# Performance work log

Hardware: AMD Instinct MI355X
Metric: run time of the kernel (lower is better)

## Reference

```python
import jax, jax.numpy as jnp
import numpy as np

B, T, L, D, H = 8, 8192, 256, 512, 8
HD = D // H  # head_dim = 64


def setup_inputs() -> dict:
    key = jax.random.key(0)
    ks = jax.random.split(key, 6)
    s = 0.02
    return {
        "x": jax.random.normal(ks[0], (B, T, D), jnp.float32),
        "query": jax.random.normal(ks[1], (B, L, D), jnp.float32),
        "Wq": jax.random.normal(ks[2], (D, D), jnp.float32) * s,
        "bq": jnp.zeros((D,), jnp.float32),
        "Wkv": jax.random.normal(ks[3], (D, 2 * D), jnp.float32) * s,
        "bkv": jnp.zeros((2 * D,), jnp.float32),
        "Wproj": jax.random.normal(ks[4], (D, D), jnp.float32) * s,
        "bproj": jnp.zeros((D,), jnp.float32),
    }


def reference(x, query, Wq, bq, Wkv, bkv, Wproj, bproj):
    scale = HD ** (-0.5)
    # projections (weights stored [in, out]; equivalent to torch Linear with W.T)
    q = (query @ Wq + bq).reshape(B, L, H, HD).transpose(0, 2, 1, 3)   # [B,H,L,hd]
    kv = (x @ Wkv + bkv).reshape(B, T, 2, H, HD)
    k = kv[:, :, 0].transpose(0, 2, 1, 3)                              # [B,H,T,hd]
    v = kv[:, :, 1].transpose(0, 2, 1, 3)                              # [B,H,T,hd]
    # scaled dot-product attention, full L x T scores as in original
    attn = jnp.einsum("bhld,bhtd->bhlt", q * scale, k)                 # [B,H,L,T]
    attn = jax.nn.softmax(attn, axis=-1)
    out = jnp.einsum("bhlt,bhtd->bhld", attn, v)                       # [B,H,L,hd]
    out = out.transpose(0, 2, 1, 3).reshape(B, L, D)
    return out @ Wproj + bproj
```

## Files before the change

kernel.cpp:

```cpp
#include <hip/hip_runtime.h>
#include <hip/hip_bf16.h>
#include <cstdint>
#include <cstddef>

typedef __bf16 bf16_t;
typedef __bf16 bf16x8 __attribute__((ext_vector_type(8)));
typedef __bf16 bf16x4 __attribute__((ext_vector_type(4)));
typedef float  f32x4  __attribute__((ext_vector_type(4)));

#define DEVI __device__ __forceinline__

constexpr int B_ = 8, T_ = 8192, L_ = 256, D_ = 512, H_ = 8, HD_ = 64;
constexpr float SCALE_LOG2E = 0.125f * 1.44269504088896340736f;
constexpr int NSPLIT = 8;

DEVI float fast_exp2(float x) {
#if __has_builtin(__builtin_amdgcn_exp2f)
  return __builtin_amdgcn_exp2f(x);
#else
  return exp2f(x);
#endif
}

DEVI void async16(void* lds_base, const void* gptr) {
#if __has_builtin(__builtin_amdgcn_global_load_lds)
  __builtin_amdgcn_global_load_lds(
      (__attribute__((address_space(1))) void*)gptr,
      (__attribute__((address_space(3))) void*)lds_base, 16, 0, 0);
#else
  ((bf16x8*)lds_base)[threadIdx.x & 63] = *(const bf16x8*)gptr;
#endif
}

__global__ __launch_bounds__(256) void cvt_f32_to_bf16(
    const float* __restrict__ in, bf16_t* __restrict__ out, int n4) {
  int stride = gridDim.x * blockDim.x;
  for (int i = blockIdx.x * blockDim.x + threadIdx.x; i < n4; i += stride) {
    float4 v = ((const float4*)in)[i];
    bf16x4 o;
    o[0] = (bf16_t)v.x; o[1] = (bf16_t)v.y; o[2] = (bf16_t)v.z; o[3] = (bf16_t)v.w;
    ((bf16x4*)out)[i] = o;
  }
}

__global__ __launch_bounds__(256) void transpose_cvt(
    const float* __restrict__ W, bf16_t* __restrict__ WT, int K, int N, float scale) {
  __shared__ float tile[32][33];
  const int tx = threadIdx.x & 31, ty = threadIdx.x >> 5;
  const int n0 = blockIdx.x * 32, k0 = blockIdx.y * 32;
#pragma unroll
  for (int i = 0; i < 4; ++i)
    tile[ty + i * 8][tx] = W[(size_t)(k0 + ty + i * 8) * N + n0 + tx];
  __syncthreads();
#pragma unroll
  for (int i = 0; i < 4; ++i)
    WT[(size_t)(n0 + ty + i * 8) * K + k0 + tx] = (bf16_t)(tile[tx][ty + i * 8] * scale);
}

template <int MODE>
__global__ __launch_bounds__(256, 4) void gemm_bf16(
    const bf16_t* __restrict__ A, const bf16_t* __restrict__ BT,
    const float* __restrict__ bias, float bscale,
    bf16_t* __restrict__ out0,
    float* __restrict__ outf) {
  constexpr int K = 512;
  __shared__ __align__(16) union SM {
    bf16_t stage[2][128 * 64];
    bf16_t cs[128 * 136];
  } sm;

  const int tid = threadIdx.x;
  const int w = tid >> 6, lane = tid & 63;
  const int m0 = blockIdx.x * 128, n0 = blockIdx.y * 128;
  const int wm = w & 1, wn = w >> 1;

  f32x4 acc[4][4] = {};

  const int sw = ((lane & 7) ^ ((lane >> 3) & 7)) * 8;
  const bf16_t* aG = A + (size_t)(m0 + w * 32 + (lane >> 3)) * K + sw;
  const bf16_t* bG = BT + (size_t)(n0 + w * 32 + (lane >> 3)) * K + sw;
  bf16_t* aL = &sm.stage[0][(w * 32) * 64];
  bf16_t* bL = &sm.stage[1][(w * 32) * 64];

  for (int k0 = 0; k0 < K; k0 += 64) {
#pragma unroll
    for (int i = 0; i < 4; ++i) {
      async16(aL + i * (8 * 64), aG + k0 + (size_t)(i * 8) * K);
      async16(bL + i * (8 * 64), bG + k0 + (size_t)(i * 8) * K);
    }
    __syncthreads();
#pragma unroll
    for (int kk = 0; kk < 2; ++kk) {
      bf16x8 af[4], bfr[4];
      const int cc = ((kk * 4 + (lane >> 4)) ^ (lane & 7)) * 8;
#pragma unroll
      for (int mt = 0; mt < 4; ++mt)
        af[mt] = *(const bf16x8*)&sm.stage[0][(wm * 64 + mt * 16 + (lane & 15)) * 64 + cc];
#pragma unroll
      for (int nt = 0; nt < 4; ++nt)
        bfr[nt] = *(const bf16x8*)&sm.stage[1][(wn * 64 + nt * 16 + (lane & 15)) * 64 + cc];
#pragma unroll
      for (int mt = 0; mt < 4; ++mt)
#pragma unroll
        for (int nt = 0; nt < 4; ++nt)
          acc[mt][nt] = __builtin_amdgcn_mfma_f32_16x16x32_bf16(af[mt], bfr[nt], acc[mt][nt], 0, 0, 0);
    }
    __syncthreads();
  }

  if (MODE == 2) {
#pragma unroll
    for (int nt = 0; nt < 4; ++nt) {
      const int col = n0 + wn * 64 + nt * 16 + (lane & 15);
      const float bv = bias[col];
#pragma unroll
      for (int mt = 0; mt < 4; ++mt)
#pragma unroll
        for (int r = 0; r < 4; ++r) {
          const int row = m0 + wm * 64 + mt * 16 + (lane >> 4) * 4 + r;
          outf[(size_t)row * D_ + col] = acc[mt][nt][r] + bv;
        }
    }
    return;
  }

#pragma unroll
  for (int nt = 0; nt < 4; ++nt) {
    const int col = wn * 64 + nt * 16 + (lane & 15);
    const float bv = bias[n0 + col] * bscale;
#pragma unroll
    for (int mt = 0; mt < 4; ++mt)
#pragma unroll
      for (int r = 0; r < 4; ++r) {
        const int row = wm * 64 + mt * 16 + (lane >> 4) * 4 + r;
        sm.cs[row * 136 + col] = (bf16_t)(acc[mt][nt][r] + bv);
      }
  }
  __syncthreads();

#pragma unroll
  for (int i = 0; i < 8; ++i) {
    const int c = tid + i * 256;
    const int row = c >> 4, col = (c & 15) * 8;
    const int gr = m0 + row;
    const int b = gr >> 8, l = gr & 255;
    const int h = (n0 + col) >> 6, hd = (n0 + col) & 63;
    *(float4*)&out0[((size_t)(b * 8 + h) * L_ + l) * 64 + hd] =
        *(const float4*)&sm.cs[row * 136 + col];
  }
}

__global__ __launch_bounds__(512, 2) void gemm_kv(
    const bf16_t* __restrict__ A, const bf16_t* __restrict__ BT,
    const float* __restrict__ bias,
    bf16_t* __restrict__ kh, bf16_t* __restrict__ vTh) {
  constexpr int K = 512;
  __shared__ __align__(16) union SM {
    bf16_t stage[2][2][256 * 64];
    bf16_t cs[128 * 264];
  } sm;

  const int tid = threadIdx.x;
  const int w = tid >> 6, lane = tid & 63;
  const int wm = w & 1, wn = w >> 1;

  const int b = blockIdx.x;
  const int xcd = b & 7, idx = b >> 3;
  const int m0 = ((xcd << 5) | (idx >> 2)) * 256;
  const int n0 = (idx & 3) * 256;

  f32x4 acc[8][4] = {};

  const int sw = ((lane & 7) ^ ((lane >> 3) & 7)) * 8;
  const int rl = w * 8 + (lane >> 3);
  const bf16_t* aG = A + (size_t)(m0 + rl) * K + sw;
  const bf16_t* bG = BT + (size_t)(n0 + rl) * K + sw;
  bf16_t* SS = &sm.stage[0][0][0];

  const int la = lane & 15;
  const int cc0 = ((lane >> 4) ^ (lane & 7)) * 8;
  const int cc1 = ((4 + (lane >> 4)) ^ (lane & 7)) * 8;

  bf16x8 ra[8], rb[4];

  auto stage_full = [&](int bufo, int k0) {
    bf16_t* dA = SS + bufo + (w * 8) * 64;
    bf16_t* dB = SS + bufo + 16384 + (w * 8) * 64;
#pragma unroll
    for (int i = 0; i < 4; ++i)
      async16(dA + i * 4096, aG + k0 + (size_t)(i * 64) * K);
#pragma unroll
    for (int i = 0; i < 4; ++i)
      async16(dB + i * 4096, bG + k0 + (size_t)(i * 64) * K);
  };
  auto ld_a = [&](const bf16_t* base, int mq) {
#pragma unroll
    for (int mt = 0; mt < 4; ++mt) {
      ra[mt * 2]     = *(const bf16x8*)&base[(mq * 64 + mt * 16 + la) * 64 + cc0];
      ra[mt * 2 + 1] = *(const bf16x8*)&base[(mq * 64 + mt * 16 + la) * 64 + cc1];
    }
  };
  auto ld_b = [&](const bf16_t* base, int nq) {
#pragma unroll
    for (int ntl = 0; ntl < 2; ++ntl) {
      rb[ntl * 2]     = *(const bf16x8*)&base[((nq * 2 + ntl) * 16 + la) * 64 + cc0];
      rb[ntl * 2 + 1] = *(const bf16x8*)&base[((nq * 2 + ntl) * 16 + la) * 64 + cc1];
    }
  };
  auto mm16 = [&](int mq, int nq) {
    __builtin_amdgcn_s_setprio(1);
#pragma unroll
    for (int mt = 0; mt < 4; ++mt)
#pragma unroll
      for (int ntl = 0; ntl < 2; ++ntl) {
        f32x4& c = acc[mq * 4 + mt][nq * 2 + ntl];
        c = __builtin_amdgcn_mfma_f32_16x16x32_bf16(ra[mt * 2],     rb[ntl * 2],     c, 0, 0, 0);
        c = __builtin_amdgcn_mfma_f32_16x16x32_bf16(ra[mt * 2 + 1], rb[ntl * 2 + 1], c, 0, 0, 0);
      }
    __builtin_amdgcn_s_setprio(0);
  };

  stage_full(0, 0);
  asm volatile("s_waitcnt vmcnt(0)" ::: "memory");
  __builtin_amdgcn_s_barrier();

#pragma unroll
  for (int t = 0; t < 8; ++t) {
    const int Xo = (t & 1) * 32768, Yo = ((t + 1) & 1) * 32768;
    const bf16_t* Ax = SS + Xo + wm * 8192;
    const bf16_t* Bx = SS + Xo + 16384 + wn * 4096;
    ld_a(Ax, 0);
    ld_b(Bx, 0);
    if (t < 7) stage_full(Yo, (t + 1) * 64);
    __builtin_amdgcn_s_barrier();
    mm16(0, 0);
    __builtin_amdgcn_s_barrier();
    ld_b(Bx, 1);
    __builtin_amdgcn_s_barrier();
    mm16(0, 1);
    __builtin_amdgcn_s_barrier();
    ld_a(Ax, 1);
    __builtin_amdgcn_s_barrier();
    mm16(1, 1);
    __builtin_amdgcn_s_barrier();
    ld_b(Bx, 0);
    __builtin_amdgcn_s_barrier();
    mm16(1, 0);
    if (t < 7) asm volatile("s_waitcnt vmcnt(0)" ::: "memory");
    __builtin_amdgcn_s_barrier();
  }
  __syncthreads();

  float bv[4];
#pragma unroll
  for (int nt = 0; nt < 4; ++nt)
    bv[nt] = bias[n0 + wn * 64 + nt * 16 + (lane & 15)];

  if (n0 < 512) {
#pragma unroll
    for (int mh = 0; mh < 2; ++mh) {
      if (wm == mh) {
#pragma unroll
        for (int a = 0; a < 8; ++a)
#pragma unroll
          for (int nt = 0; nt < 4; ++nt)
#pragma unroll
            for (int r = 0; r < 4; ++r) {
              const int rowL = a * 16 + (lane >> 4) * 4 + r;
              const int col = wn * 64 + nt * 16 + (lane & 15);
              sm.cs[rowL * 264 + col] = (bf16_t)(acc[a][nt][r] + bv[nt]);
            }
      }
      __syncthreads();
#pragma unroll
      for (int i = 0; i < 8; ++i) {
        const int c = tid + i * 512;
        const int row = c >> 5, col = (c & 31) * 8;
        const int gr = m0 + mh * 128 + row;
        const int bb = gr >> 13, tt = gr & 8191;
        const int h = (n0 + col) >> 6, hd = (n0 + col) & 63;
        *(float4*)&kh[((size_t)(bb * 8 + h) * T_ + tt) * 64 + hd] =
            *(const float4*)&sm.cs[row * 264 + col];
      }
      __syncthreads();
    }
  } else {
    const int bb = m0 >> 13, t0 = m0 & 8191;
#pragma unroll
    for (int nh = 0; nh < 2; ++nh) {
      if ((wn >> 1) == nh) {
#pragma unroll
        for (int a = 0; a < 8; ++a)
#pragma unroll
          for (int nt = 0; nt < 4; ++nt)
#pragma unroll
            for (int r = 0; r < 4; ++r) {
              const int row = wm * 128 + a * 16 + (lane >> 4) * 4 + r;
              const int colL = (wn & 1) * 64 + nt * 16 + (lane & 15);
              sm.cs[colL * 264 + row] = (bf16_t)(acc[a][nt][r] + bv[nt]);
            }
      }
      __syncthreads();
#pragma unroll
      for (int i = 0; i < 8; ++i) {
        const int c = tid + i * 512;
        const int colL = c >> 5, tb = (c & 31) * 8;
        const int ch = (n0 - 512) + nh * 128 + colL;
        const int h = ch >> 6, hd = ch & 63;
        *(float4*)&vTh[((size_t)(bb * 8 + h) * 64 + hd) * T_ + t0 + tb] =
            *(const float4*)&sm.cs[colL * 264 + tb];
      }
      __syncthreads();
    }
  }
}

__global__ __launch_bounds__(256, 4) void attn_fwd(
    const bf16_t* __restrict__ qg, const bf16_t* __restrict__ kg,
    const bf16_t* __restrict__ vg, float* __restrict__ Opart,
    float* __restrict__ lbuf) {
  __shared__ __align__(16) bf16_t KPs[10240];
  __shared__ __align__(16) bf16_t Vs[4 * 64 * 32];
  bf16_t* Ks = KPs;
  bf16_t* Ps = KPs;
  bf16_t* Qs = KPs;

  const int n = blockIdx.x;
  const int split = n & 7, qt = (n >> 3) & 3, bh = n >> 5;
  const int tid = threadIdx.x;
  const int w = tid >> 6, lane = tid & 63;

  {
    const bf16_t* src = qg + ((size_t)bh * L_ + qt * 64) * 64;
    const int row = w * 16 + (lane >> 2);
#pragma unroll
    for (int hh = 0; hh < 2; ++hh)
      async16(&Qs[hh * 2048 + (w * 16) * 32],
              src + (size_t)row * 64 + hh * 32 + (lane & 3) * 8);
  }
  __syncthreads();

  bf16x8 aq[2];
#pragma unroll
  for (int hh = 0; hh < 2; ++hh)
    aq[hh] = *(const bf16x8*)&Qs[hh * 2048 + (w * 16 + (lane & 15)) * 32 + (lane >> 4) * 8];
  __syncthreads();

  bf16x8 ones;
#pragma unroll
  for (int j = 0; j < 8; ++j) ones[j] = (bf16_t)1.0f;

  f32x4 O[4] = {};
  f32x4 lacc = {0.f, 0.f, 0.f, 0.f};

  const int kt0 = split * (T_ / 128 / NSPLIT);
  for (int kt = kt0; kt < kt0 + T_ / 128 / NSPLIT; ++kt) {
#pragma unroll
    for (int hh = 0; hh < 2; ++hh)
#pragma unroll
      for (int i = 0; i < 2; ++i) {
        const int trow = kt * 128 + w * 32 + i * 16 + (lane >> 2);
        async16(&Ks[hh * 4096 + (w * 32 + i * 16) * 32],
                kg + ((size_t)bh * T_ + trow) * 64 + hh * 32 + (lane & 3) * 8);
      }
#pragma unroll
    for (int kc = 0; kc < 4; ++kc) {
      const int hd = w * 16 + (lane >> 2);
      async16(&Vs[kc * 2048 + (w * 16) * 32],
              vg + ((size_t)bh * 64 + hd) * T_ + kt * 128 + kc * 32 + (lane & 3) * 8);
    }
    __syncthreads();

    f32x4 S[8];
#pragma unroll
    for (int nt = 0; nt < 8; ++nt) {
      bf16x8 b0 = *(const bf16x8*)&Ks[0 * 4096 + (nt * 16 + (lane & 15)) * 32 + (lane >> 4) * 8];
      bf16x8 b1 = *(const bf16x8*)&Ks[1 * 4096 + (nt * 16 + (lane & 15)) * 32 + (lane >> 4) * 8];
      f32x4 s = {0.f, 0.f, 0.f, 0.f};
      s = __builtin_amdgcn_mfma_f32_16x16x32_bf16(aq[0], b0, s, 0, 0, 0);
      s = __builtin_amdgcn_mfma_f32_16x16x32_bf16(aq[1], b1, s, 0, 0, 0);
#pragma unroll
      for (int r = 0; r < 4; ++r) s[r] = fast_exp2(s[r]);
      S[nt] = s;
    }

    __syncthreads();

#pragma unroll
    for (int nt = 0; nt < 8; ++nt)
#pragma unroll
      for (int r = 0; r < 4; ++r) {
        const int rp = w * 16 + (lane >> 4) * 4 + r;
        Ps[(nt >> 1) * 2560 + rp * 40 + (nt & 1) * 16 + (lane & 15)] = (bf16_t)S[nt][r];
      }

    __syncthreads();

#pragma unroll
    for (int kc = 0; kc < 4; ++kc) {
      bf16x8 ap = *(const bf16x8*)&Ps[kc * 2560 + (w * 16 + (lane & 15)) * 40 + (lane >> 4) * 8];
      lacc = __builtin_amdgcn_mfma_f32_16x16x32_bf16(ap, ones, lacc, 0, 0, 0);
#pragma unroll
      for (int n2 = 0; n2 < 4; ++n2) {
        bf16x8 bv = *(const bf16x8*)&Vs[kc * 2048 + (n2 * 16 + (lane & 15)) * 32 + (lane >> 4) * 8];
        O[n2] = __builtin_amdgcn_mfma_f32_16x16x32_bf16(ap, bv, O[n2], 0, 0, 0);
      }
    }
    __syncthreads();
  }

  const int part = ((bh * 4 + qt) * NSPLIT + split);
  float* op = Opart + (size_t)part * 64 * 64;
#pragma unroll
  for (int n2 = 0; n2 < 4; ++n2) {
#pragma unroll
    for (int r = 0; r < 4; ++r) {
      const int row = w * 16 + (lane >> 4) * 4 + r;
      op[(size_t)row * 64 + n2 * 16 + (lane & 15)] = O[n2][r];
    }
  }
  if ((lane & 15) == 0) {
    float* lb = lbuf + (size_t)part * 64;
#pragma unroll
    for (int r = 0; r < 4; ++r)
      lb[w * 16 + (lane >> 4) * 4 + r] = lacc[r];
  }
}

__global__ __launch_bounds__(256) void attn_combine(
    const float* __restrict__ Opart, const float* __restrict__ lbuf,
    bf16_t* __restrict__ og) {
  const int blk = blockIdx.x;
  const int bh = blk >> 2, qt = blk & 3;
  const int tid = threadIdx.x;
  const int row = tid >> 2, c0 = (tid & 3) * 16;
  float L = 0.f;
#pragma unroll
  for (int s = 0; s < NSPLIT; ++s) L += lbuf[((size_t)blk * NSPLIT + s) * 64 + row];
  const float inv = 1.f / L;
  f32x4 acc[4] = {};
  const float* ob = Opart + (size_t)blk * NSPLIT * 4096 + row * 64 + c0;
#pragma unroll
  for (int s = 0; s < NSPLIT; ++s)
#pragma unroll
    for (int j = 0; j < 4; ++j) {
      f32x4 v = *(const f32x4*)&ob[s * 4096 + j * 4];
      acc[j] += v;
    }
  const int b = bh >> 3, h = bh & 7;
  bf16_t* dst = og + ((size_t)(b * L_ + qt * 64 + row)) * D_ + h * 64 + c0;
#pragma unroll
  for (int j = 0; j < 4; ++j) {
    bf16x4 o;
#pragma unroll
    for (int e = 0; e < 4; ++e) o[e] = (bf16_t)(acc[j][e] * inv);
    *(bf16x4*)&dst[j * 4] = o;
  }
}

extern "C" void kernel_launch(void* const* d_in, const int* in_sizes, int n_in,
                              void* d_out, int out_size, void* d_ws, size_t ws_size,
                              hipStream_t stream) {
  const float* x     = (const float*)d_in[0];
  const float* query = (const float*)d_in[1];
  const float* Wq    = (const float*)d_in[2];
  const float* bq    = (const float*)d_in[3];
  const float* Wkv   = (const float*)d_in[4];
  const float* bkv   = (const float*)d_in[5];
  const float* Wproj = (const float*)d_in[6];
  const float* bproj = (const float*)d_in[7];
  float* out = (float*)d_out;

  char* ws = (char*)d_ws;
  bf16_t* xb   = (bf16_t*)(ws + 0);
  float*  Opart = (float*)(ws + 0);
  float*  lbuf  = (float*)(ws + 34603008);
  bf16_t* wkvT = (bf16_t*)(ws + 67108864);
  bf16_t* wqT  = (bf16_t*)(ws + 68157440);
  bf16_t* qin  = (bf16_t*)(ws + 68681728);
  bf16_t* qh   = (bf16_t*)(ws + 70778880);
  bf16_t* kh   = (bf16_t*)(ws + 72876032);
  bf16_t* vTh  = (bf16_t*)(ws + 139984896);
  bf16_t* attnb = (bf16_t*)(ws + 207093760);
  bf16_t* wprojT = (bf16_t*)(ws + 209190912);

  cvt_f32_to_bf16<<<4096, 256, 0, stream>>>(x, xb, (B_ * T_ * D_) / 4);
  cvt_f32_to_bf16<<<1024, 256, 0, stream>>>(query, qin, (B_ * L_ * D_) / 4);
  transpose_cvt<<<dim3(16, 16), 256, 0, stream>>>(Wq, wqT, 512, 512, SCALE_LOG2E);
  transpose_cvt<<<dim3(32, 16), 256, 0, stream>>>(Wkv, wkvT, 512, 1024, 1.0f);
  transpose_cvt<<<dim3(16, 16), 256, 0, stream>>>(Wproj, wprojT, 512, 512, 1.0f);
  gemm_bf16<0><<<dim3(16, 4), 256, 0, stream>>>(qin, wqT, bq, SCALE_LOG2E, qh, nullptr);
  gemm_kv<<<dim3(1024), 512, 0, stream>>>(xb, wkvT, bkv, kh, vTh);
  attn_fwd<<<dim3(64 * 4 * NSPLIT), 256, 0, stream>>>(qh, kh, vTh, Opart, lbuf);
  attn_combine<<<dim3(256), 256, 0, stream>>>(Opart, lbuf, attnb);
  gemm_bf16<2><<<dim3(16, 4), 256, 0, stream>>>(attnb, wprojT, bproj, 1.0f, nullptr, out);
}
```

Before: 390.3 us.

## Split GEMM tile staging into halves with partial vmcnt waits

Each K-step's async global-to-LDS staging is split into two halves, issued at different points in the MFMA schedule. The LDS row layout of A and B is remapped so the first half holds exactly the rows used by the first quadrant computations. The full vmcnt(0) drain becomes vmcnt(4), so only the needed half is waited for while the rest stays in flight. This aims to overlap more memory latency with compute, but the fine-grained wait counting is fragile and could race if the issue order is wrong.

```diff
diff --git a/kernel.cpp b/kernel.cpp
--- a/kernel.cpp
+++ b/kernel.cpp
@@ -172,9 +172,8 @@
   f32x4 acc[8][4] = {};
 
   const int sw = ((lane & 7) ^ ((lane >> 3) & 7)) * 8;
-  const int rl = w * 8 + (lane >> 3);
-  const bf16_t* aG = A + (size_t)(m0 + rl) * K + sw;
-  const bf16_t* bG = BT + (size_t)(n0 + rl) * K + sw;
+  const bf16_t* aG = A + (size_t)(m0 + w * 8 + (lane >> 3)) * K + sw;
+  const bf16_t* bG = BT + (size_t)(n0 + (lane >> 3)) * K + sw;
   bf16_t* SS = &sm.stage[0][0][0];
 
   const int la = lane & 15;
@@ -183,28 +182,37 @@
 
   bf16x8 ra[8], rb[4];
 
-  auto stage_full = [&](int bufo, int k0) {
+  auto stage_A_half = [&](int bufo, int k0, int h) {
     bf16_t* dA = SS + bufo + (w * 8) * 64;
+    const int gb0 = (h == 0) ? 0 : 1;
+    const int gb1 = (h == 0) ? 2 : 3;
+    async16(dA + (h * 2 + 0) * 4096, aG + k0 + (size_t)(gb0 * 64) * K);
+    async16(dA + (h * 2 + 1) * 4096, aG + k0 + (size_t)(gb1 * 64) * K);
+  };
+  auto stage_B_half = [&](int bufo, int k0, int h) {
     bf16_t* dB = SS + bufo + 16384 + (w * 8) * 64;
 #pragma unroll
-    for (int i = 0; i < 4; ++i)
-      async16(dA + i * 4096, aG + k0 + (size_t)(i * 64) * K);
-#pragma unroll
-    for (int i = 0; i < 4; ++i)
-      async16(dB + i * 4096, bG + k0 + (size_t)(i * 64) * K);
+    for (int j = 0; j < 2; ++j) {
+      const int i = h * 2 + j;
+      const int r0 = i * 64 + w * 8;
+      const int g0 = ((r0 & 127) >> 5) * 64 + (r0 & 31) + (r0 >> 7) * 32;
+      async16(dB + i * 4096, bG + k0 + (size_t)g0 * K);
+    }
   };
-  auto ld_a = [&](const bf16_t* base, int mq) {
+  auto ld_a = [&](const bf16_t* Abase, int mq) {
 #pragma unroll
     for (int mt = 0; mt < 4; ++mt) {
-      ra[mt * 2]     = *(const bf16x8*)&base[(mq * 64 + mt * 16 + la) * 64 + cc0];
-      ra[mt * 2 + 1] = *(const bf16x8*)&base[(mq * 64 + mt * 16 + la) * 64 + cc1];
+      const int rp = mq * 128 + wm * 64 + mt * 16 + la;
+      ra[mt * 2]     = *(const bf16x8*)&Abase[rp * 64 + cc0];
+      ra[mt * 2 + 1] = *(const bf16x8*)&Abase[rp * 64 + cc1];
     }
   };
-  auto ld_b = [&](const bf16_t* base, int nq) {
+  auto ld_b = [&](const bf16_t* Bbase, int nq) {
 #pragma unroll
     for (int ntl = 0; ntl < 2; ++ntl) {
-      rb[ntl * 2]     = *(const bf16x8*)&base[((nq * 2 + ntl) * 16 + la) * 64 + cc0];
-      rb[ntl * 2 + 1] = *(const bf16x8*)&base[((nq * 2 + ntl) * 16 + la) * 64 + cc1];
+      const int rp = nq * 128 + wn * 32 + ntl * 16 + la;
+      rb[ntl * 2]     = *(const bf16x8*)&Bbase[rp * 64 + cc0];
+      rb[ntl * 2 + 1] = *(const bf16x8*)&Bbase[rp * 64 + cc1];
     }
   };
   auto mm16 = [&](int mq, int nq) {
@@ -220,22 +228,26 @@
     __builtin_amdgcn_s_setprio(0);
   };
 
-  stage_full(0, 0);
-  asm volatile("s_waitcnt vmcnt(0)" ::: "memory");
+  stage_A_half(0, 0, 0); stage_B_half(0, 0, 0);
+  stage_A_half(0, 0, 1); stage_B_half(0, 0, 1);
+  asm volatile("s_waitcnt vmcnt(4)" ::: "memory");
   __builtin_amdgcn_s_barrier();
 
 #pragma unroll
   for (int t = 0; t < 8; ++t) {
     const int Xo = (t & 1) * 32768, Yo = ((t + 1) & 1) * 32768;
-    const bf16_t* Ax = SS + Xo + wm * 8192;
-    const bf16_t* Bx = SS + Xo + 16384 + wn * 4096;
+    const bf16_t* Ax = SS + Xo;
+    const bf16_t* Bx = SS + Xo + 16384;
     ld_a(Ax, 0);
     ld_b(Bx, 0);
-    if (t < 7) stage_full(Yo, (t + 1) * 64);
+    if (t < 7) { stage_A_half(Yo, (t + 1) * 64, 0); stage_B_half(Yo, (t + 1) * 64, 0); }
     __builtin_amdgcn_s_barrier();
     mm16(0, 0);
+    if (t < 7) asm volatile("s_waitcnt vmcnt(4)" ::: "memory");
+    else       asm volatile("s_waitcnt vmcnt(0)" ::: "memory");
     __builtin_amdgcn_s_barrier();
     ld_b(Bx, 1);
+    if (t < 7) { stage_A_half(Yo, (t + 1) * 64, 1); stage_B_half(Yo, (t + 1) * 64, 1); }
     __builtin_amdgcn_s_barrier();
     mm16(0, 1);
     __builtin_amdgcn_s_barrier();
@@ -246,7 +258,7 @@
     ld_b(Bx, 0);
     __builtin_amdgcn_s_barrier();
     mm16(1, 0);
-    if (t < 7) asm volatile("s_waitcnt vmcnt(0)" ::: "memory");
+    if (t < 7) asm volatile("s_waitcnt vmcnt(4)" ::: "memory");
     __builtin_amdgcn_s_barrier();
   }
   __syncthreads();
```

Result: no change. 389.5 us (-0.2%).
